# Performance work log

Measured on AMD Instinct MI355X. Metric: run time of the kernel, lower is better.

The kernel has to match this reference:

```python
import math
import jax, jax.numpy as jnp
import numpy as np

SEGMENT_LENGTHS = [1024, 2048, 4096]
DILATION_RATES = [1, 2, 4]


def _head_groups(num_heads, num_segments):
    base = num_heads // num_segments
    extra = num_heads % num_segments
    groups = [base] * num_segments
    for i in range(extra):
        groups[-(i + 1)] += 1
    return groups


def _dilated_indices(n, segment_len, dilation_rate, offset):
    # Mirrors RingDilatedAttentionV3._apply_dilated_pattern (static shapes -> numpy)
    if dilation_rate == 1:
        return np.arange(n, dtype=np.int32)
    out = []
    for start in range(0, n, segment_len):
        seg = np.arange(start, min(start + segment_len, n), dtype=np.int32)
        if len(seg) >= dilation_rate:
            dil = seg[offset::dilation_rate]
            while len(dil) < len(seg):
                dil = np.concatenate([dil, seg[: len(seg) - len(dil)]])
            out.append(dil[: len(seg)])
        else:
            out.append(seg)
    return np.concatenate(out)


def _build_head_indices(n, h):
    # [h, n] gather indices along the sequence dim, one row per head
    groups = _head_groups(h, len(SEGMENT_LENGTHS))
    rows = []
    for i, (s, r, g) in enumerate(zip(SEGMENT_LENGTHS, DILATION_RATES, groups)):
        idx = _dilated_indices(n, s, r, offset=i)
        rows.extend([idx] * g)
    return np.stack(rows)


def setup_inputs() -> dict:
    key = jax.random.key(0)
    kq, kk, kv = jax.random.split(key, 3)
    b, n, h, d = 1, 4096, 12, 64
    q = jax.random.normal(kq, (b, n, h, d), dtype=jnp.float32)
    k = jax.random.normal(kk, (b, n, h, d), dtype=jnp.float32)
    v = jax.random.normal(kv, (b, n, h, d), dtype=jnp.float32)
    return {"q": q, "k": k, "v": v}


def reference(q, k, v):
    b, n, h, d = q.shape
    idx = jnp.asarray(_build_head_indices(n, h))  # [h, n], static

    # (b, n, h, d) -> (b, h, n, d)
    qt = jnp.transpose(q, (0, 2, 1, 3))
    kt = jnp.transpose(k, (0, 2, 1, 3))
    vt = jnp.transpose(v, (0, 2, 1, 3))

    # Dilated gather along sequence, per head
    gather_idx = idx[None, :, :, None]  # [1, h, n, 1]
    kt = jnp.take_along_axis(kt, gather_idx, axis=2)
    vt = jnp.take_along_axis(vt, gather_idx, axis=2)

    scale = 1.0 / math.sqrt(d)
    scores = jnp.einsum("bhqd,bhkd->bhqk", qt, kt) * scale  # [b, h, n, n]
    attn = jax.nn.softmax(scores, axis=-1)
    out = jnp.einsum("bhqk,bhkd->bhqd", attn, vt)
    return jnp.transpose(out, (0, 2, 1, 3))  # (b, n, h, d)
```

## Files before the change

### kernel.cpp

```cpp
#include <hip/hip_runtime.h>
#include <hip/hip_bf16.h>
#include <math.h>


#define NQ 4096
#define NH 12
#define DD 64
#define KV 64
#define NT (NQ / KV)
#define STRD 36

#define EXP2 __builtin_amdgcn_exp2f

typedef __attribute__((ext_vector_type(8))) short bf16x8;
typedef __attribute__((ext_vector_type(4))) float f32x4;

__device__ __forceinline__ int map_src(int h, int j) {
    if (h < 4) {
        return j;
    } else if (h < 8) {
        int p = j & 2047;
        int base = j & ~2047;
        return base + (p < 1024 ? 1 + 2 * p : p - 1024);
    } else {
        return (j < 1024) ? (2 + 4 * j) : (j - 1024);
    }
}

__device__ __forceinline__ unsigned pk2(float lo, float hi) {
    __hip_bfloat162 t = __float22bfloat162_rn(float2{lo, hi});
    union { __hip_bfloat162 h; unsigned u; } c;
    c.h = t;
    return c.u;
}

__device__ __forceinline__ int swz(int row, int p) {
    return row * STRD + (p ^ (((row >> 2) & 7) << 2));
}

struct Pre {
    float4 kq[4];
    float4 va[2], vb[2];
};

__global__ __launch_bounds__(256, 2) void attn_mfma(
    const float* __restrict__ q,
    const float* __restrict__ k,
    const float* __restrict__ v,
    float* __restrict__ out)
{
    __shared__ __align__(16) unsigned short KsB[2][KV * STRD * 2];
    __shared__ __align__(16) unsigned short VtB[2][DD * STRD * 2];
    __shared__ __align__(16) unsigned short Ps[4 * 16 * STRD * 2];

    const int h    = blockIdx.y;
    const int qblk = blockIdx.x;
    const int tid  = threadIdx.x;
    const int wave = tid >> 6;
    const int lane = tid & 63;
    const int lq   = lane & 15;
    const int g    = lane >> 4;

    const int qi   = qblk * 64 + wave * 16 + lq;
    const int keyK = tid >> 4;
    const int pV   = tid >> 4;
    const int c4   = (tid & 15) << 2;

    int offK[4], offV[4];
    auto recompute = [&](int t) {
        const int j0 = t * KV;
        #pragma unroll
        for (int i = 0; i < 4; ++i)
            offK[i] = (map_src(h, j0 + keyK + 16 * i) * NH + h) * DD;
        offV[0] = (map_src(h, j0 + 2 * pV)      * NH + h) * DD;
        offV[1] = (map_src(h, j0 + 2 * pV + 1)  * NH + h) * DD;
        offV[2] = (map_src(h, j0 + 2 * pV + 32) * NH + h) * DD;
        offV[3] = (map_src(h, j0 + 2 * pV + 33) * NH + h) * DD;
    };
    auto advance = [&](int T) {
        if ((T & 15) == 0) { recompute(T); return; }
        int d;
        if (h < 4)      d = 64;
        else if (h < 8) d = (((T * KV) & 2047) < 1024) ? 128 : 64;
        else            d = (T < 16) ? 256 : 64;
        d *= NH * DD;
        #pragma unroll
        for (int i = 0; i < 4; ++i) offK[i] += d;
        #pragma unroll
        for (int i = 0; i < 4; ++i) offV[i] += d;
    };

    auto stage_load = [&](Pre& pr) {
        #pragma unroll
        for (int i = 0; i < 4; ++i)
            pr.kq[i] = *(const float4*)(k + offK[i] + c4);
        pr.va[0] = *(const float4*)(v + offV[0] + c4);
        pr.vb[0] = *(const float4*)(v + offV[1] + c4);
        pr.va[1] = *(const float4*)(v + offV[2] + c4);
        pr.vb[1] = *(const float4*)(v + offV[3] + c4);
    };
    auto stage_write = [&](unsigned short* Ks, unsigned* Vw, const Pre& pr) {
        #pragma unroll
        for (int i = 0; i < 4; ++i) {
            uint2 w;
            w.x = pk2(pr.kq[i].x, pr.kq[i].y);
            w.y = pk2(pr.kq[i].z, pr.kq[i].w);
            *(uint2*)((char*)Ks + (keyK + 16 * i) * (STRD * 4) + c4 * 2) = w;
        }
        #pragma unroll
        for (int i = 0; i < 2; ++i) {
            int p = pV + 16 * i;
            Vw[swz(c4 + 0, p)] = pk2(pr.va[i].x, pr.vb[i].x);
            Vw[swz(c4 + 1, p)] = pk2(pr.va[i].y, pr.vb[i].y);
            Vw[swz(c4 + 2, p)] = pk2(pr.va[i].z, pr.vb[i].z);
            Vw[swz(c4 + 3, p)] = pk2(pr.va[i].w, pr.vb[i].w);
        }
    };

    const float qscale = 0.125f * 1.4426950408889634f;
    union { bf16x8 v8; unsigned u[4]; } qf[2];
    {
        const float* qp = q + (qi * NH + h) * DD;
        #pragma unroll
        for (int ks = 0; ks < 2; ++ks) {
            float4 a = *(const float4*)(qp + 32 * ks + 8 * g);
            float4 b = *(const float4*)(qp + 32 * ks + 8 * g + 4);
            qf[ks].u[0] = pk2(a.x * qscale, a.y * qscale);
            qf[ks].u[1] = pk2(a.z * qscale, a.w * qscale);
            qf[ks].u[2] = pk2(b.x * qscale, b.y * qscale);
            qf[ks].u[3] = pk2(b.z * qscale, b.w * qscale);
        }
    }

    f32x4 o[4];
    #pragma unroll
    for (int mf = 0; mf < 4; ++mf) o[mf] = f32x4{0.f, 0.f, 0.f, 0.f};
    float m = -INFINITY, l = 0.f;

    unsigned* Pw = (unsigned*)Ps + wave * 16 * STRD;

    Pre pr;
    recompute(0);
    stage_load(pr);
    stage_write(KsB[0], (unsigned*)VtB[0], pr);

    for (int tile = 0; tile < NT; ++tile) {
        const int cur = tile & 1;
        __syncthreads();

        if (tile + 1 < NT) { advance(tile + 1); stage_load(pr); }

        const unsigned short* Ksc = KsB[cur];
        const unsigned short* Vtc = VtB[cur];

        f32x4 s[4];
        #pragma unroll
        for (int mf = 0; mf < 4; ++mf) {
            s[mf] = f32x4{0.f, 0.f, 0.f, 0.f};
            #pragma unroll
            for (int ks = 0; ks < 2; ++ks) {
                bf16x8 kf = *(const bf16x8*)(Ksc + (16 * mf + lq) * (STRD * 2) + 8 * g + 32 * ks);
                s[mf] = __builtin_amdgcn_mfma_f32_16x16x32_bf16(kf, qf[ks].v8, s[mf], 0, 0, 0);
            }
        }

        float u0 = fmaxf(fmaxf(s[0].x, s[0].y), s[0].z);
        float u1 = fmaxf(fmaxf(s[0].w, s[1].x), s[1].y);
        float u2 = fmaxf(fmaxf(s[1].z, s[1].w), s[2].x);
        float u3 = fmaxf(fmaxf(s[2].y, s[2].z), s[2].w);
        float u4 = fmaxf(fmaxf(s[3].x, s[3].y), s[3].z);
        float tm = fmaxf(fmaxf(fmaxf(u0, u1), u2),
                         fmaxf(fmaxf(u3, u4), s[3].w));
        tm = fmaxf(tm, __shfl_xor(tm, 16));
        tm = fmaxf(tm, __shfl_xor(tm, 32));
        if (__any(tm > m)) {
            float mn = fmaxf(m, tm);
            float sc = EXP2(m - mn);
            m = mn;
            l *= sc;
            #pragma unroll
            for (int mf = 0; mf < 4; ++mf) o[mf] *= sc;
        }
        #pragma unroll
        for (int mf = 0; mf < 4; ++mf) {
            f32x4 p;
            p.x = EXP2(s[mf].x - m);
            p.y = EXP2(s[mf].y - m);
            p.z = EXP2(s[mf].z - m);
            p.w = EXP2(s[mf].w - m);
            l += (p.x + p.y) + (p.z + p.w);
            Pw[swz(lq, 8 * mf + 2 * g + 0)] = pk2(p.x, p.y);
            Pw[swz(lq, 8 * mf + 2 * g + 1)] = pk2(p.z, p.w);
        }

        bf16x8 pf0 = *(const bf16x8*)((const unsigned short*)(Pw + swz(lq, 4 * g)));
        bf16x8 pf1 = *(const bf16x8*)((const unsigned short*)(Pw + swz(lq, 4 * g + 16)));
        #pragma unroll
        for (int mf = 0; mf < 4; ++mf) {
            const int vr = 16 * mf + lq;
            bf16x8 vf0 = *(const bf16x8*)(Vtc + 2 * swz(vr, 4 * g));
            o[mf] = __builtin_amdgcn_mfma_f32_16x16x32_bf16(vf0, pf0, o[mf], 0, 0, 0);
            bf16x8 vf1 = *(const bf16x8*)(Vtc + 2 * swz(vr, 4 * g + 16));
            o[mf] = __builtin_amdgcn_mfma_f32_16x16x32_bf16(vf1, pf1, o[mf], 0, 0, 0);
        }

        if (tile + 1 < NT) stage_write(KsB[cur ^ 1], (unsigned*)VtB[cur ^ 1], pr);
    }

    l += __shfl_xor(l, 16);
    l += __shfl_xor(l, 32);
    float inv = 1.f / l;
    float* op = out + (qi * NH + h) * DD;
    #pragma unroll
    for (int mf = 0; mf < 4; ++mf) {
        f32x4 r = o[mf] * inv;
        *(f32x4*)(op + 16 * mf + 4 * g) = r;
    }
}

extern "C" void kernel_launch(void* const* d_in, const int* in_sizes, int n_in,
                              void* d_out, int out_size, void* d_ws, size_t ws_size,
                              hipStream_t stream) {
    const float* q = (const float*)d_in[0];
    const float* k = (const float*)d_in[1];
    const float* v = (const float*)d_in[2];
    float* out     = (float*)d_out;

    dim3 grid(NQ / 64, NH);
    attn_mfma<<<grid, 256, 0, stream>>>(q, k, v, out);
}
```

Before: 195.8 us.

## Prepack K/V into swizzled bf16 tiles and stream them via global_load_lds

Adds a prepack kernel that gathers the dilated K/V rows once, converts them to bf16, transposes V, and stores swizzled 64x64 tiles in the workspace. The attention kernel then copies each tile straight into LDS with async global_load_lds, so it no longer does per-block fp32 loads, conversions and scattered LDS writes. The goal is less global traffic (bf16, computed once instead of per query block) and more overlap between loads and MFMA work. The cost is an extra kernel launch and a workspace round trip. Correctness also depends on the LDS async load and the barrier ordering being right, since there is no explicit wait counter.

```diff
diff --git a/kernel.cpp b/kernel.cpp
--- a/kernel.cpp
+++ b/kernel.cpp
@@ -8,12 +8,14 @@
 #define DD 64
 #define KV 64
 #define NT (NQ / KV)
-#define STRD 36
-
+#define PSTR 36
+#define TILE_USHORT (KV * DD)
+#define TILE_BYTES  (KV * DD * 2)
 #define EXP2 __builtin_amdgcn_exp2f
 
 typedef __attribute__((ext_vector_type(8))) short bf16x8;
 typedef __attribute__((ext_vector_type(4))) float f32x4;
+typedef __attribute__((ext_vector_type(4))) unsigned int u32x4;
 
 __device__ __forceinline__ int map_src(int h, int j) {
     if (h < 4) {
@@ -35,23 +37,73 @@
 }
 
 __device__ __forceinline__ int swz(int row, int p) {
-    return row * STRD + (p ^ (((row >> 2) & 7) << 2));
-}
-
-struct Pre {
-    float4 kq[4];
-    float4 va[2], vb[2];
-};
+    return row * PSTR + (p ^ (((row >> 2) & 7) << 2));
+}
+
+__device__ __forceinline__ void gload16(const void* g, void* l) {
+    __builtin_amdgcn_global_load_lds(
+        (const __attribute__((address_space(1))) unsigned int*)g,
+        (__attribute__((address_space(3))) unsigned int*)l, 16, 0, 0);
+}
+
+__global__ __launch_bounds__(256) void prepack(
+    const float* __restrict__ k, const float* __restrict__ v,
+    unsigned short* __restrict__ kp, unsigned short* __restrict__ vp)
+{
+    __shared__ float vt[KV][DD + 1];
+    const int t = blockIdx.x, h = blockIdx.y, tid = threadIdx.x;
+    const int row = tid >> 2, q4 = tid & 3;
+    const int src = map_src(h, t * KV + row);
+
+    {
+        const float* kr = k + ((size_t)src * NH + h) * DD + 16 * q4;
+        float4 a = *(const float4*)(kr + 0);
+        float4 b = *(const float4*)(kr + 4);
+        float4 c = *(const float4*)(kr + 8);
+        float4 d = *(const float4*)(kr + 12);
+        unsigned* kb = (unsigned*)(kp + (size_t)(h * NT + t) * TILE_USHORT);
+        const int x = (row & 7) << 2;
+        u32x4 w0, w1;
+        w0.x = pk2(a.x, a.y); w0.y = pk2(a.z, a.w);
+        w0.z = pk2(b.x, b.y); w0.w = pk2(b.z, b.w);
+        w1.x = pk2(c.x, c.y); w1.y = pk2(c.z, c.w);
+        w1.z = pk2(d.x, d.y); w1.w = pk2(d.z, d.w);
+        *(u32x4*)(kb + (row << 5) + ((8 * q4) ^ x))     = w0;
+        *(u32x4*)(kb + (row << 5) + ((8 * q4 + 4) ^ x)) = w1;
+    }
+    {
+        const float* vr = v + ((size_t)src * NH + h) * DD + 16 * q4;
+        #pragma unroll
+        for (int i = 0; i < 16; ++i) vt[row][16 * q4 + i] = vr[i];
+    }
+    __syncthreads();
+    {
+        const int d = row, u = q4;
+        unsigned* vb = (unsigned*)(vp + (size_t)(h * NT + t) * TILE_USHORT);
+        const int x = (d & 7) << 2;
+        u32x4 w0, w1;
+        w0.x = pk2(vt[16*u +  0][d], vt[16*u +  1][d]);
+        w0.y = pk2(vt[16*u +  2][d], vt[16*u +  3][d]);
+        w0.z = pk2(vt[16*u +  4][d], vt[16*u +  5][d]);
+        w0.w = pk2(vt[16*u +  6][d], vt[16*u +  7][d]);
+        w1.x = pk2(vt[16*u +  8][d], vt[16*u +  9][d]);
+        w1.y = pk2(vt[16*u + 10][d], vt[16*u + 11][d]);
+        w1.z = pk2(vt[16*u + 12][d], vt[16*u + 13][d]);
+        w1.w = pk2(vt[16*u + 14][d], vt[16*u + 15][d]);
+        *(u32x4*)(vb + (d << 5) + ((8 * u) ^ x))     = w0;
+        *(u32x4*)(vb + (d << 5) + ((8 * u + 4) ^ x)) = w1;
+    }
+}
 
 __global__ __launch_bounds__(256, 2) void attn_mfma(
     const float* __restrict__ q,
-    const float* __restrict__ k,
-    const float* __restrict__ v,
+    const unsigned short* __restrict__ kp,
+    const unsigned short* __restrict__ vp,
     float* __restrict__ out)
 {
-    __shared__ __align__(16) unsigned short KsB[2][KV * STRD * 2];
-    __shared__ __align__(16) unsigned short VtB[2][DD * STRD * 2];
-    __shared__ __align__(16) unsigned short Ps[4 * 16 * STRD * 2];
+    __shared__ __align__(16) unsigned short KsB[2][TILE_USHORT];
+    __shared__ __align__(16) unsigned short VtB[2][TILE_USHORT];
+    __shared__ __align__(16) unsigned short Ps[4 * 16 * PSTR * 2];
 
     const int h    = blockIdx.y;
     const int qblk = blockIdx.x;
@@ -60,67 +112,19 @@
     const int lane = tid & 63;
     const int lq   = lane & 15;
     const int g    = lane >> 4;
-
-    const int qi   = qblk * 64 + wave * 16 + lq;
-    const int keyK = tid >> 4;
-    const int pV   = tid >> 4;
-    const int c4   = (tid & 15) << 2;
-
-    int offK[4], offV[4];
-    auto recompute = [&](int t) {
-        const int j0 = t * KV;
-        #pragma unroll
-        for (int i = 0; i < 4; ++i)
-            offK[i] = (map_src(h, j0 + keyK + 16 * i) * NH + h) * DD;
-        offV[0] = (map_src(h, j0 + 2 * pV)      * NH + h) * DD;
-        offV[1] = (map_src(h, j0 + 2 * pV + 1)  * NH + h) * DD;
-        offV[2] = (map_src(h, j0 + 2 * pV + 32) * NH + h) * DD;
-        offV[3] = (map_src(h, j0 + 2 * pV + 33) * NH + h) * DD;
-    };
-    auto advance = [&](int T) {
-        if ((T & 15) == 0) { recompute(T); return; }
-        int d;
-        if (h < 4)      d = 64;
-        else if (h < 8) d = (((T * KV) & 2047) < 1024) ? 128 : 64;
-        else            d = (T < 16) ? 256 : 64;
-        d *= NH * DD;
-        #pragma unroll
-        for (int i = 0; i < 4; ++i) offK[i] += d;
-        #pragma unroll
-        for (int i = 0; i < 4; ++i) offV[i] += d;
-    };
-
-    auto stage_load = [&](Pre& pr) {
-        #pragma unroll
-        for (int i = 0; i < 4; ++i)
-            pr.kq[i] = *(const float4*)(k + offK[i] + c4);
-        pr.va[0] = *(const float4*)(v + offV[0] + c4);
-        pr.vb[0] = *(const float4*)(v + offV[1] + c4);
-        pr.va[1] = *(const float4*)(v + offV[2] + c4);
-        pr.vb[1] = *(const float4*)(v + offV[3] + c4);
-    };
-    auto stage_write = [&](unsigned short* Ks, unsigned* Vw, const Pre& pr) {
-        #pragma unroll
-        for (int i = 0; i < 4; ++i) {
-            uint2 w;
-            w.x = pk2(pr.kq[i].x, pr.kq[i].y);
-            w.y = pk2(pr.kq[i].z, pr.kq[i].w);
-            *(uint2*)((char*)Ks + (keyK + 16 * i) * (STRD * 4) + c4 * 2) = w;
-        }
-        #pragma unroll
-        for (int i = 0; i < 2; ++i) {
-            int p = pV + 16 * i;
-            Vw[swz(c4 + 0, p)] = pk2(pr.va[i].x, pr.vb[i].x);
-            Vw[swz(c4 + 1, p)] = pk2(pr.va[i].y, pr.vb[i].y);
-            Vw[swz(c4 + 2, p)] = pk2(pr.va[i].z, pr.vb[i].z);
-            Vw[swz(c4 + 3, p)] = pk2(pr.va[i].w, pr.vb[i].w);
-        }
-    };
+    const int xk   = (lq & 7) << 2;
+
+    const int qi = qblk * 64 + wave * 16 + lq;
+
+    const char* ksrc = (const char*)(kp + (size_t)h * NT * TILE_USHORT);
+    const char* vsrc = (const char*)(vp + (size_t)h * NT * TILE_USHORT);
+    const int lbase = wave * 2048;
+    const int csrc  = lbase + lane * 16;
 
     const float qscale = 0.125f * 1.4426950408889634f;
     union { bf16x8 v8; unsigned u[4]; } qf[2];
     {
-        const float* qp = q + (qi * NH + h) * DD;
+        const float* qp = q + ((size_t)qi * NH + h) * DD;
         #pragma unroll
         for (int ks = 0; ks < 2; ++ks) {
             float4 a = *(const float4*)(qp + 32 * ks + 8 * g);
@@ -137,18 +141,24 @@
     for (int mf = 0; mf < 4; ++mf) o[mf] = f32x4{0.f, 0.f, 0.f, 0.f};
     float m = -INFINITY, l = 0.f;
 
-    unsigned* Pw = (unsigned*)Ps + wave * 16 * STRD;
-
-    Pre pr;
-    recompute(0);
-    stage_load(pr);
-    stage_write(KsB[0], (unsigned*)VtB[0], pr);
+    unsigned* Pw = (unsigned*)Ps + wave * 16 * PSTR;
+
+    gload16(ksrc + csrc,        (char*)KsB[0] + lbase);
+    gload16(ksrc + csrc + 1024, (char*)KsB[0] + lbase + 1024);
+    gload16(vsrc + csrc,        (char*)VtB[0] + lbase);
+    gload16(vsrc + csrc + 1024, (char*)VtB[0] + lbase + 1024);
 
     for (int tile = 0; tile < NT; ++tile) {
         const int cur = tile & 1;
         __syncthreads();
 
-        if (tile + 1 < NT) { advance(tile + 1); stage_load(pr); }
+        if (tile + 1 < NT) {
+            const size_t nb = (size_t)(tile + 1) * TILE_BYTES;
+            gload16(ksrc + nb + csrc,        (char*)KsB[cur ^ 1] + lbase);
+            gload16(ksrc + nb + csrc + 1024, (char*)KsB[cur ^ 1] + lbase + 1024);
+            gload16(vsrc + nb + csrc,        (char*)VtB[cur ^ 1] + lbase);
+            gload16(vsrc + nb + csrc + 1024, (char*)VtB[cur ^ 1] + lbase + 1024);
+        }
 
         const unsigned short* Ksc = KsB[cur];
         const unsigned short* Vtc = VtB[cur];
@@ -159,7 +169,7 @@
             s[mf] = f32x4{0.f, 0.f, 0.f, 0.f};
             #pragma unroll
             for (int ks = 0; ks < 2; ++ks) {
-                bf16x8 kf = *(const bf16x8*)(Ksc + (16 * mf + lq) * (STRD * 2) + 8 * g + 32 * ks);
+                bf16x8 kf = *(const bf16x8*)(Ksc + 2 * (((16 * mf + lq) << 5) + ((4 * g + 16 * ks) ^ xk)));
                 s[mf] = __builtin_amdgcn_mfma_f32_16x16x32_bf16(kf, qf[ks].v8, s[mf], 0, 0, 0);
             }
         }
@@ -198,19 +208,17 @@
         #pragma unroll
         for (int mf = 0; mf < 4; ++mf) {
             const int vr = 16 * mf + lq;
-            bf16x8 vf0 = *(const bf16x8*)(Vtc + 2 * swz(vr, 4 * g));
+            bf16x8 vf0 = *(const bf16x8*)(Vtc + 2 * ((vr << 5) + ((4 * g) ^ xk)));
             o[mf] = __builtin_amdgcn_mfma_f32_16x16x32_bf16(vf0, pf0, o[mf], 0, 0, 0);
-            bf16x8 vf1 = *(const bf16x8*)(Vtc + 2 * swz(vr, 4 * g + 16));
+            bf16x8 vf1 = *(const bf16x8*)(Vtc + 2 * ((vr << 5) + ((4 * g + 16) ^ xk)));
             o[mf] = __builtin_amdgcn_mfma_f32_16x16x32_bf16(vf1, pf1, o[mf], 0, 0, 0);
         }
-
-        if (tile + 1 < NT) stage_write(KsB[cur ^ 1], (unsigned*)VtB[cur ^ 1], pr);
     }
 
     l += __shfl_xor(l, 16);
     l += __shfl_xor(l, 32);
     float inv = 1.f / l;
-    float* op = out + (qi * NH + h) * DD;
+    float* op = out + ((size_t)qi * NH + h) * DD;
     #pragma unroll
     for (int mf = 0; mf < 4; ++mf) {
         f32x4 r = o[mf] * inv;
@@ -226,6 +234,9 @@
     const float* v = (const float*)d_in[2];
     float* out     = (float*)d_out;
 
-    dim3 grid(NQ / 64, NH);
-    attn_mfma<<<grid, 256, 0, stream>>>(q, k, v, out);
-}
+    unsigned short* kp = (unsigned short*)d_ws;
+    unsigned short* vp = kp + (size_t)NH * NT * TILE_USHORT;
+
+    prepack<<<dim3(NT, NH), 256, 0, stream>>>(k, v, kp, vp);
+    attn_mfma<<<dim3(NQ / 64, NH), 256, 0, stream>>>(q, kp, vp, out);
+}
```

Measured after the change: 178.7 us. -8.7%, faster.
